# Optimization experiments

Measured on AMD Instinct MI355X. Metric: run time of the kernel, lower is better.

## Reference

```python
import jax, jax.numpy as jnp
import numpy as np

N_FEATURES = 4096
N_ACTIONS = 4
N_CLAUSES_PER_ACTION = 10
N_CLAUSES = N_ACTIONS * N_CLAUSES_PER_ACTION
BATCH = 16384
EPS = 1e-8
ACTIVE_THRESH = 1e-6


def setup_inputs() -> dict:
    key = jax.random.key(0)
    k1, k2, k3, k4 = jax.random.split(key, 4)
    features = jax.random.uniform(k1, (BATCH, N_FEATURES), dtype=jnp.float32)
    # nn.Parameter(torch.randn(F, C) * 2.0)
    clause_weights = jax.random.normal(k2, (N_FEATURES, N_CLAUSES), dtype=jnp.float32) * 2.0
    # nn.Parameter(torch.randn(F, C) * 0.5 + 2.0)
    mask_logits = jax.random.normal(k3, (N_FEATURES, N_CLAUSES), dtype=jnp.float32) * 0.5 + 2.0
    # gumbel/concrete uniform noise (torch.rand_like(mask_logits)), fixed for determinism
    u = jax.random.uniform(k4, (N_FEATURES, N_CLAUSES), dtype=jnp.float32)
    temperature = jnp.float32(5.0)
    return {"features": features, "clause_weights": clause_weights,
            "mask_logits": mask_logits, "u": u, "temperature": temperature}


def reference(features, clause_weights, mask_logits, u, temperature):
    # --- sample_mask (training: concrete relaxation) ---
    s = jax.nn.sigmoid((jnp.log(u + EPS) - jnp.log(1.0 - u + EPS) + mask_logits)
                       / (temperature + EPS))                     # (F, C)
    # --- get_clause_weights (training: soft ternary * mask) ---
    w = jnp.tanh(clause_weights / (temperature + EPS)) * s        # (F, C)

    # --- evaluate all clauses at once (masked literal mean) ---
    # literal = where(w > 0, x, 1 - x), restricted to active features (|w| > 1e-6).
    # sum_f active*literal = x @ A_pos + (1 - x) @ A_neg, so no (B,F,C) intermediate.
    active = jnp.abs(w) > ACTIVE_THRESH
    pos = (active & (w > 0)).astype(features.dtype)               # (F, C)
    neg = (active & ~(w > 0)).astype(features.dtype)              # (F, C)
    num = features @ pos + (1.0 - features) @ neg                 # (B, C)
    cnt = pos.sum(axis=0) + neg.sum(axis=0)                       # (C,)
    # mean over active literals; empty clause -> satisfaction 1
    sat = jnp.where(cnt > 0, num / jnp.maximum(cnt, 1.0), 1.0)    # (B, C)

    # --- per-action segment sum (assignment = arange(C) // cpa, contiguous) ---
    B = features.shape[0]
    action_scores = sat.reshape(B, N_ACTIONS, N_CLAUSES_PER_ACTION).sum(axis=-1)
    return action_scores                                          # (B, n_actions)
```

## Files before the change

kernel.cpp:

```cpp
#include <hip/hip_runtime.h>
#include <hip/hip_bf16.h>

#define N_FEATURES 4096
#define N_ACTIONS 4
#define N_CPA 10
#define N_CLAUSES 40
#define BATCH 16384
#define EPS 1e-8f
#define ACTIVE_THRESH 1e-6f

typedef float f4v __attribute__((ext_vector_type(4)));

__global__ void clause_kernel(const float* __restrict__ cw,
                              const float* __restrict__ ml,
                              const float* __restrict__ u,
                              const float* __restrict__ tptr,
                              float* __restrict__ d,
                              float* __restrict__ cnt,
                              float* __restrict__ negcnt)
{
    const int c = blockIdx.x;
    const float temp = tptr[0] + EPS;
    const float invt = 1.0f / temp;

    float pcount = 0.0f, ncount = 0.0f;
    for (int f = threadIdx.x; f < N_FEATURES; f += 512) {
        const int idx = f * N_CLAUSES + c;
        float uu = u[idx];
        float z = (__logf((uu + EPS) / (1.0f - uu + EPS)) + ml[idx]) * invt;
        float s = 1.0f / (1.0f + __expf(-z));
        float w = tanhf(cw[idx] * invt) * s;
        bool active = fabsf(w) > ACTIVE_THRESH;
        bool pos = active && (w > 0.0f);
        bool neg = active && !(w > 0.0f);
        d[c * N_FEATURES + f] = pos ? 1.0f : (neg ? -1.0f : 0.0f);
        pcount += pos ? 1.0f : 0.0f;
        ncount += neg ? 1.0f : 0.0f;
    }

    #pragma unroll
    for (int off = 32; off; off >>= 1) {
        pcount += __shfl_down(pcount, off);
        ncount += __shfl_down(ncount, off);
    }
    __shared__ float sp[8], sn[8];
    const int wave = threadIdx.x >> 6;
    const int lane = threadIdx.x & 63;
    if (lane == 0) { sp[wave] = pcount; sn[wave] = ncount; }
    __syncthreads();
    if (threadIdx.x == 0) {
        float P = 0.0f, Nn = 0.0f;
        #pragma unroll
        for (int w8 = 0; w8 < 8; ++w8) { P += sp[w8]; Nn += sn[w8]; }
        cnt[c] = P + Nn;
        negcnt[c] = Nn;
    }
}

__global__ void dmat_kernel(const float* __restrict__ d,
                            const float* __restrict__ cnt,
                            const float* __restrict__ negcnt,
                            float* __restrict__ D,
                            float* __restrict__ K)
{
    const int idx = blockIdx.x * blockDim.x + threadIdx.x;
    const int f = idx & (N_FEATURES - 1);
    const int a = idx >> 12;
    float acc = 0.0f;
    #pragma unroll
    for (int j = 0; j < N_CPA; ++j) {
        const int c = a * N_CPA + j;
        float cn = cnt[c];
        float inv = (cn > 0.0f) ? (1.0f / cn) : 0.0f;
        acc += d[c * N_FEATURES + f] * inv;
    }
    D[a * N_FEATURES + f] = acc;
    if (idx < N_ACTIONS) {
        float k = 0.0f;
        #pragma unroll
        for (int j = 0; j < N_CPA; ++j) {
            const int c = idx * N_CPA + j;
            float cn = cnt[c];
            k += (cn > 0.0f) ? (negcnt[c] / cn) : 1.0f;
        }
        K[idx] = k;
    }
}

#define RPB 8

__global__ __launch_bounds__(256, 3) void gemv_kernel(const float* __restrict__ x,
                                                      const float* __restrict__ D,
                                                      const float* __restrict__ K,
                                                      float* __restrict__ out)
{
    const int tid  = threadIdx.x;
    const int wave = tid >> 6;
    const int lane = tid & 63;

    __shared__ float red[4][32];

    f4v Dr[4][4];
    #pragma unroll
    for (int c = 0; c < 4; ++c)
        #pragma unroll
        for (int a = 0; a < 4; ++a)
            Dr[c][a] = *(const f4v*)(D + a * N_FEATURES + (c * 256 + tid) * 4);

    const int rb = blockIdx.x * RPB;
    const f4v* xrow = (const f4v*)(x + (size_t)rb * N_FEATURES);

    float acc[RPB][4];
    #pragma unroll
    for (int r = 0; r < RPB; ++r)
        #pragma unroll
        for (int a = 0; a < 4; ++a) acc[r][a] = 0.0f;

    f4v xv[2][4];
    #pragma unroll
    for (int c = 0; c < 4; ++c)
        xv[0][c] = __builtin_nontemporal_load(&xrow[c * 256 + tid]);

    #pragma unroll
    for (int r = 0; r < RPB; ++r) {
        const int cur = r & 1, nxt = cur ^ 1;
        if (r + 1 < RPB) {
            #pragma unroll
            for (int c = 0; c < 4; ++c)
                xv[nxt][c] = __builtin_nontemporal_load(&xrow[(r + 1) * 1024 + c * 256 + tid]);
        }
        #pragma unroll
        for (int c = 0; c < 4; ++c) {
            const f4v xc = xv[cur][c];
            #pragma unroll
            for (int a = 0; a < 4; ++a)
                acc[r][a] += xc.x * Dr[c][a].x + xc.y * Dr[c][a].y
                           + xc.z * Dr[c][a].z + xc.w * Dr[c][a].w;
        }
    }

    #pragma unroll
    for (int off = 32; off; off >>= 1)
        #pragma unroll
        for (int r = 0; r < RPB; ++r)
            #pragma unroll
            for (int a = 0; a < 4; ++a)
                acc[r][a] += __shfl_xor(acc[r][a], off);

    float myv = acc[0][0];
    #pragma unroll
    for (int v = 1; v < 32; ++v)
        if (lane == v) myv = acc[v >> 2][v & 3];
    if (lane < 32) red[wave][lane] = myv;
    __syncthreads();

    if (tid < 32) {
        float s = red[0][tid] + red[1][tid] + red[2][tid] + red[3][tid];
        out[rb * N_ACTIONS + tid] = s + K[tid & 3];
    }
}

extern "C" void kernel_launch(void* const* d_in, const int* in_sizes, int n_in,
                              void* d_out, int out_size, void* d_ws, size_t ws_size,
                              hipStream_t stream) {
    const float* features = (const float*)d_in[0];
    const float* cw       = (const float*)d_in[1];
    const float* ml       = (const float*)d_in[2];
    const float* u        = (const float*)d_in[3];
    const float* tptr     = (const float*)d_in[4];
    float* out = (float*)d_out;

    float* ws = (float*)d_ws;
    float* d_buf   = ws;
    float* cnt     = d_buf + N_CLAUSES * N_FEATURES;
    float* negcnt  = cnt + N_CLAUSES;
    float* Dmat    = negcnt + N_CLAUSES;
    float* K       = Dmat + N_ACTIONS * N_FEATURES;

    clause_kernel<<<N_CLAUSES, 512, 0, stream>>>(cw, ml, u, tptr, d_buf, cnt, negcnt);
    dmat_kernel<<<(N_ACTIONS * N_FEATURES) / 256, 256, 0, stream>>>(d_buf, cnt, negcnt, Dmat, K);
    gemv_kernel<<<BATCH / RPB, 256, 0, stream>>>(features, Dmat, K, out);
}
```

Measured before the change: 60.42 us.

## Restructure mask preprocessing into per-feature count and fold kernels with recompute

Replaces the per-clause kernel, which read the (F,C) parameter arrays with a stride of 40 floats, by a per-feature kernel that loads each feature's 40 clause values as float4 vectors and counts positive and negative literals with wave ballots. A second kernel recomputes the mask per feature and folds it straight into the per-action D matrix and the K offsets. This drops the 40x4096 intermediate sign buffer and its reread. The cost is evaluating the transcendental mask math twice and running only 16 blocks per preprocessing kernel.

```diff
diff --git a/kernel.cpp b/kernel.cpp
--- a/kernel.cpp
+++ b/kernel.cpp
@@ -11,79 +11,116 @@
 
 typedef float f4v __attribute__((ext_vector_type(4)));
 
-__global__ void clause_kernel(const float* __restrict__ cw,
-                              const float* __restrict__ ml,
-                              const float* __restrict__ u,
-                              const float* __restrict__ tptr,
-                              float* __restrict__ d,
-                              float* __restrict__ cnt,
-                              float* __restrict__ negcnt)
+__device__ __forceinline__ void compute_w4(const float4 u4, const float4 m4,
+                                           const float4 c4, const float invt,
+                                           bool pos[4], bool neg[4]) {
+    const float uu[4] = {u4.x, u4.y, u4.z, u4.w};
+    const float mm[4] = {m4.x, m4.y, m4.z, m4.w};
+    const float ww[4] = {c4.x, c4.y, c4.z, c4.w};
+    #pragma unroll
+    for (int e = 0; e < 4; ++e) {
+        float z = (__logf((uu[e] + EPS) / (1.0f - uu[e] + EPS)) + mm[e]) * invt;
+        float s = 1.0f / (1.0f + __expf(-z));
+        float w = tanhf(ww[e] * invt) * s;
+        bool active = fabsf(w) > ACTIVE_THRESH;
+        pos[e] = active && (w > 0.0f);
+        neg[e] = active && !(w > 0.0f);
+    }
+}
+
+__global__ void count_kernel(const float* __restrict__ cw,
+                             const float* __restrict__ ml,
+                             const float* __restrict__ u,
+                             const float* __restrict__ tptr,
+                             float* __restrict__ part_pos,
+                             float* __restrict__ part_neg)
 {
-    const int c = blockIdx.x;
-    const float temp = tptr[0] + EPS;
-    const float invt = 1.0f / temp;
-
-    float pcount = 0.0f, ncount = 0.0f;
-    for (int f = threadIdx.x; f < N_FEATURES; f += 512) {
-        const int idx = f * N_CLAUSES + c;
-        float uu = u[idx];
-        float z = (__logf((uu + EPS) / (1.0f - uu + EPS)) + ml[idx]) * invt;
-        float s = 1.0f / (1.0f + __expf(-z));
-        float w = tanhf(cw[idx] * invt) * s;
-        bool active = fabsf(w) > ACTIVE_THRESH;
-        bool pos = active && (w > 0.0f);
-        bool neg = active && !(w > 0.0f);
-        d[c * N_FEATURES + f] = pos ? 1.0f : (neg ? -1.0f : 0.0f);
-        pcount += pos ? 1.0f : 0.0f;
-        ncount += neg ? 1.0f : 0.0f;
-    }
-
-    #pragma unroll
-    for (int off = 32; off; off >>= 1) {
-        pcount += __shfl_down(pcount, off);
-        ncount += __shfl_down(ncount, off);
-    }
-    __shared__ float sp[8], sn[8];
-    const int wave = threadIdx.x >> 6;
-    const int lane = threadIdx.x & 63;
-    if (lane == 0) { sp[wave] = pcount; sn[wave] = ncount; }
+    __shared__ float spw[4][N_CLAUSES], snw[4][N_CLAUSES];
+    const int tid = threadIdx.x, wave = tid >> 6, lane = tid & 63;
+    const int f = blockIdx.x * 256 + tid;
+    const float invt = 1.0f / (tptr[0] + EPS);
+
+    const float4* ub = (const float4*)(u  + (size_t)f * N_CLAUSES);
+    const float4* mb = (const float4*)(ml + (size_t)f * N_CLAUSES);
+    const float4* cb = (const float4*)(cw + (size_t)f * N_CLAUSES);
+
+    #pragma unroll
+    for (int cq = 0; cq < N_CLAUSES / 4; ++cq) {
+        bool pos[4], neg[4];
+        compute_w4(ub[cq], mb[cq], cb[cq], invt, pos, neg);
+        #pragma unroll
+        for (int e = 0; e < 4; ++e) {
+            unsigned long long bp = __ballot(pos[e]);
+            unsigned long long bn = __ballot(neg[e]);
+            if (lane == 0) {
+                spw[wave][cq * 4 + e] = (float)__popcll(bp);
+                snw[wave][cq * 4 + e] = (float)__popcll(bn);
+            }
+        }
+    }
     __syncthreads();
-    if (threadIdx.x == 0) {
-        float P = 0.0f, Nn = 0.0f;
-        #pragma unroll
-        for (int w8 = 0; w8 < 8; ++w8) { P += sp[w8]; Nn += sn[w8]; }
-        cnt[c] = P + Nn;
-        negcnt[c] = Nn;
-    }
-}
-
-__global__ void dmat_kernel(const float* __restrict__ d,
-                            const float* __restrict__ cnt,
-                            const float* __restrict__ negcnt,
+    if (tid < N_CLAUSES) {
+        float p = spw[0][tid] + spw[1][tid] + spw[2][tid] + spw[3][tid];
+        float n = snw[0][tid] + snw[1][tid] + snw[2][tid] + snw[3][tid];
+        part_pos[blockIdx.x * N_CLAUSES + tid] = p;
+        part_neg[blockIdx.x * N_CLAUSES + tid] = n;
+    }
+}
+
+__global__ void fold_kernel(const float* __restrict__ cw,
+                            const float* __restrict__ ml,
+                            const float* __restrict__ u,
+                            const float* __restrict__ tptr,
+                            const float* __restrict__ part_pos,
+                            const float* __restrict__ part_neg,
                             float* __restrict__ D,
                             float* __restrict__ K)
 {
-    const int idx = blockIdx.x * blockDim.x + threadIdx.x;
-    const int f = idx & (N_FEATURES - 1);
-    const int a = idx >> 12;
-    float acc = 0.0f;
-    #pragma unroll
-    for (int j = 0; j < N_CPA; ++j) {
-        const int c = a * N_CPA + j;
-        float cn = cnt[c];
-        float inv = (cn > 0.0f) ? (1.0f / cn) : 0.0f;
-        acc += d[c * N_FEATURES + f] * inv;
-    }
-    D[a * N_FEATURES + f] = acc;
-    if (idx < N_ACTIONS) {
+    __shared__ float sinv[N_CLAUSES], sneg[N_CLAUSES];
+    const int tid = threadIdx.x;
+    if (tid < N_CLAUSES) {
+        float p = 0.0f, n = 0.0f;
+        #pragma unroll
+        for (int b = 0; b < 16; ++b) {
+            p += part_pos[b * N_CLAUSES + tid];
+            n += part_neg[b * N_CLAUSES + tid];
+        }
+        float cn = p + n;
+        sinv[tid] = (cn > 0.0f) ? (1.0f / cn) : 0.0f;
+        sneg[tid] = n;
+    }
+    __syncthreads();
+
+    const int f = blockIdx.x * 256 + tid;
+    const float invt = 1.0f / (tptr[0] + EPS);
+    const float4* ub = (const float4*)(u  + (size_t)f * N_CLAUSES);
+    const float4* mb = (const float4*)(ml + (size_t)f * N_CLAUSES);
+    const float4* cb = (const float4*)(cw + (size_t)f * N_CLAUSES);
+
+    float acc[N_ACTIONS] = {0.0f, 0.0f, 0.0f, 0.0f};
+    #pragma unroll
+    for (int cq = 0; cq < N_CLAUSES / 4; ++cq) {
+        bool pos[4], neg[4];
+        compute_w4(ub[cq], mb[cq], cb[cq], invt, pos, neg);
+        #pragma unroll
+        for (int e = 0; e < 4; ++e) {
+            const int c = cq * 4 + e;
+            float d = pos[e] ? 1.0f : (neg[e] ? -1.0f : 0.0f);
+            acc[c / N_CPA] += d * sinv[c];
+        }
+    }
+    #pragma unroll
+    for (int a = 0; a < N_ACTIONS; ++a)
+        D[a * N_FEATURES + f] = acc[a];
+
+    if (blockIdx.x == 0 && tid < N_ACTIONS) {
         float k = 0.0f;
         #pragma unroll
         for (int j = 0; j < N_CPA; ++j) {
-            const int c = idx * N_CPA + j;
-            float cn = cnt[c];
-            k += (cn > 0.0f) ? (negcnt[c] / cn) : 1.0f;
-        }
-        K[idx] = k;
+            const int c = tid * N_CPA + j;
+            k += (sinv[c] > 0.0f) ? (sneg[c] * sinv[c]) : 1.0f;
+        }
+        K[tid] = k;
     }
 }
 
@@ -171,13 +208,12 @@
     float* out = (float*)d_out;
 
     float* ws = (float*)d_ws;
-    float* d_buf   = ws;
-    float* cnt     = d_buf + N_CLAUSES * N_FEATURES;
-    float* negcnt  = cnt + N_CLAUSES;
-    float* Dmat    = negcnt + N_CLAUSES;
-    float* K       = Dmat + N_ACTIONS * N_FEATURES;
-
-    clause_kernel<<<N_CLAUSES, 512, 0, stream>>>(cw, ml, u, tptr, d_buf, cnt, negcnt);
-    dmat_kernel<<<(N_ACTIONS * N_FEATURES) / 256, 256, 0, stream>>>(d_buf, cnt, negcnt, Dmat, K);
+    float* Dmat     = ws;
+    float* K        = Dmat + N_ACTIONS * N_FEATURES;
+    float* part_pos = K + 4;
+    float* part_neg = part_pos + 16 * N_CLAUSES;
+
+    count_kernel<<<16, 256, 0, stream>>>(cw, ml, u, tptr, part_pos, part_neg);
+    fold_kernel<<<16, 256, 0, stream>>>(cw, ml, u, tptr, part_pos, part_neg, Dmat, K);
     gemv_kernel<<<BATCH / RPB, 256, 0, stream>>>(features, Dmat, K, out);
 }
```

After: 79.19 us. 31.1% more time.
